# Performance work log

Measured on AMD Instinct MI355X. Metric: run time of the kernel, lower is better.

Reference implementation:

```python
import jax, jax.numpy as jnp
import numpy as np

# ---- static HashEncoder config (matches __init__ defaults) ----
D = 3            # input_dim
L = 16           # num_levels
C = 2            # level_dim
BASE = 16.0      # base_resolution (isotropic)
SCALE = 2.0      # per_level_scale (isotropic)
MAX_PARAMS = 2 ** 19  # log2_hashmap_size = 19

_base = np.full(D, BASE, dtype=np.float64)
_pls = np.full(D, SCALE, dtype=np.float64)
_offsets = [0]
_res = []
_off = 0
for i in range(L):
    r = np.ceil(_base * _pls ** i)
    _res.append(r.astype(np.int64))
    _off += int(min(MAX_PARAMS, np.prod(r)))
    _offsets.append(_off)
TOTAL_PARAMS = _off  # 7,114,752

# spatial-hash primes (instant-ngp convention; prime for dim 0 is 1)
PRIMES = np.array([1, 2654435761, 805459861], dtype=np.uint32)
# corner bit patterns for the 2^D = 8 cube corners, shape [8, D]
BITS = np.array([[(c >> d) & 1 for d in range(D)] for c in range(2 ** D)], dtype=np.uint32)
BITS_MASK = BITS.astype(bool)


def _encode_level(x01, embeddings, l):
    """x01: [B, D] normalized coords in [0, 1]; returns [B, C]."""
    scale = (_base * _pls ** l - 1.0).astype(np.float32)        # per-dim grid scale
    res = _res[l]                                               # per-dim resolution
    level_size = _offsets[l + 1] - _offsets[l]
    pos = x01 * scale + 0.5                                     # [B, D]
    pos_grid = jnp.floor(pos)
    frac = pos - pos_grid                                       # [B, D] in [0,1)
    pg = pos_grid.astype(jnp.uint32)                            # [B, D]
    corners = pg[:, None, :] + BITS[None]                       # [B, 8, D]
    # trilinear weights: prod over dims of frac (bit=1) or 1-frac (bit=0)
    w = jnp.prod(jnp.where(BITS_MASK[None], frac[:, None, :], 1.0 - frac[:, None, :]), axis=-1)  # [B, 8]
    if int(np.prod(res)) > level_size:
        # hashed level: xor of per-dim (coord * prime), mod table size
        h = corners * PRIMES[None, None, :]
        idx = (h[..., 0] ^ h[..., 1] ^ h[..., 2]) % jnp.uint32(level_size)
    else:
        # dense level: row-major stride indexing
        stride = np.array([1, res[0], res[0] * res[1]], dtype=np.uint32)
        idx = jnp.sum(corners * stride[None, None, :], axis=-1)  # [B, 8]
    g = embeddings[_offsets[l] + idx.astype(jnp.int32)]          # [B, 8, C] gather
    return jnp.sum(w[..., None] * g, axis=1)                     # [B, C]


def setup_inputs() -> dict:
    key = jax.random.key(0)
    k1, k2 = jax.random.split(key)
    B = 1048576
    inputs = jax.random.uniform(k1, (B, D), dtype=jnp.float32, minval=-1.0, maxval=1.0)
    # reset_parameters(): uniform(-0.1, 0.1)
    embeddings = jax.random.uniform(k2, (TOTAL_PARAMS, C), dtype=jnp.float32, minval=-0.1, maxval=0.1)
    return {"inputs": inputs, "embeddings": embeddings}


def reference(inputs, embeddings):
    # forward(inputs, size=1): normalize [-1,1] -> [0,1]
    x01 = (inputs + 1.0) * 0.5
    outs = [_encode_level(x01, embeddings, l) for l in range(L)]
    return jnp.concatenate(outs, axis=-1)  # [B, L*C] = [B, 32]
```

## Files before the change

kernel.cpp:

```cpp
#include <hip/hip_runtime.h>


static constexpr uint32_t P1 = 2654435761u;
static constexpr uint32_t P2 = 805459861u;
static constexpr uint32_t NPARAMS = 7114752u;
static constexpr uint32_t HMASK = 524287u;

__device__ inline uint32_t bf16_bits(float f) {
    uint32_t u = __float_as_uint(f);
    return (u + 0x7FFFu + ((u >> 16) & 1u)) >> 16;
}

__global__ __launch_bounds__(256) void convert_bf16(
    const float* __restrict__ emb, uint32_t* __restrict__ tab)
{
    const uint32_t i = blockIdx.x * 256u + threadIdx.x;
    const float4 v = ((const float4*)emb)[i];
    uint2 o;
    o.x = bf16_bits(v.x) | (bf16_bits(v.y) << 16);
    o.y = bf16_bits(v.z) | (bf16_bits(v.w) << 16);
    ((uint2*)tab)[i] = o;
}

__global__ __launch_bounds__(256) void enc_level(
    const float* __restrict__ inp,
    const uint32_t* __restrict__ tab,
    float2* __restrict__ stage,
    int npoints)
{
    const uint32_t l = blockIdx.y;
    const uint32_t p = blockIdx.x * 256u + threadIdx.x;
    if (p >= (uint32_t)npoints) return;

    const float x01 = (inp[p * 3u + 0u] + 1.0f) * 0.5f;
    const float y01 = (inp[p * 3u + 1u] + 1.0f) * 0.5f;
    const float z01 = (inp[p * 3u + 2u] + 1.0f) * 0.5f;

    const uint32_t res = 16u << l;
    const float scale = (float)(res - 1u);

    const float posx = x01 * scale + 0.5f;
    const float posy = y01 * scale + 0.5f;
    const float posz = z01 * scale + 0.5f;

    const float fgx = floorf(posx), fgy = floorf(posy), fgz = floorf(posz);
    const float fx = posx - fgx, fy = posy - fgy, fz = posz - fgz;
    const uint32_t gx = (uint32_t)fgx, gy = (uint32_t)fgy, gz = (uint32_t)fgz;

    uint32_t off;
    if (l >= 3u)      off = 299008u + (l - 3u) * 524288u;
    else if (l == 2u) off = 36864u;
    else if (l == 1u) off = 4096u;
    else              off = 0u;
    const bool hashed = (l >= 3u);
    const uint32_t s = 4u + (hashed ? 0u : l);

    const float wx0 = 1.0f - fx, wx1 = fx;
    const float wy[2] = {1.0f - fy, fy};
    const float wz[2] = {1.0f - fz, fz};

    uint32_t yzc[4];
    if (hashed) {
        const uint32_t hy0 = gy * P1, hy1 = hy0 + P1;
        const uint32_t hz0 = gz * P2, hz1 = hz0 + P2;
        yzc[0] = hy0 ^ hz0; yzc[1] = hy1 ^ hz0;
        yzc[2] = hy0 ^ hz1; yzc[3] = hy1 ^ hz1;
    } else {
        const uint32_t dy0 = gy << s, dy1 = dy0 + (1u << s);
        const uint32_t dz0 = gz << (2u * s), dz1 = dz0 + (1u << (2u * s));
        yzc[0] = dy0 + dz0; yzc[1] = dy1 + dz0;
        yzc[2] = dy0 + dz1; yzc[3] = dy1 + dz1;
    }

    const bool gx_odd = (gx & 1u) != 0u;

    uint32_t idxA[4], idxB[4];
#pragma unroll
    for (int c = 0; c < 4; ++c) {
        if (hashed) {
            idxA[c] = (gx ^ yzc[c]) & HMASK;
            idxB[c] = ((gx + 1u) ^ yzc[c]) & HMASK;
        } else {
            idxA[c] = gx + yzc[c];
            idxB[c] = idxA[c] + 1u;
        }
    }

    uint2 pr[4];
#pragma unroll
    for (int c = 0; c < 4; ++c)
        pr[c] = *(const uint2*)(tab + off + (idxA[c] & ~1u));

    uint32_t vBo[4];
    if (gx_odd) {
#pragma unroll
        for (int c = 0; c < 4; ++c)
            vBo[c] = tab[off + idxB[c]];
    }

    float sx = 0.0f, sy = 0.0f;
#pragma unroll
    for (int c = 0; c < 4; ++c) {
        const uint32_t lo = idxA[c] & 1u;
        const uint32_t vA = lo ? pr[c].y : pr[c].x;
        const uint32_t vBe = lo ? pr[c].x : pr[c].y;
        const uint32_t vB = gx_odd ? vBo[c] : vBe;
        const float wyz = wy[c & 1] * wz[c >> 1];
        const float eAx = __uint_as_float(vA << 16);
        const float eAy = __uint_as_float(vA & 0xFFFF0000u);
        const float eBx = __uint_as_float(vB << 16);
        const float eBy = __uint_as_float(vB & 0xFFFF0000u);
        sx = fmaf(wyz, fmaf(wx0, eAx, wx1 * eBx), sx);
        sy = fmaf(wyz, fmaf(wx0, eAy, wx1 * eBy), sy);
    }

    stage[(size_t)l * (uint32_t)npoints + p] = make_float2(sx, sy);
}

__global__ __launch_bounds__(256) void transpose_out(
    const float2* __restrict__ stage, float4* __restrict__ out4, int npoints)
{
    __shared__ float2 t[256][17];
    const uint32_t p0 = blockIdx.x * 256u;
    const uint32_t tid = threadIdx.x;

#pragma unroll
    for (int l = 0; l < 16; ++l)
        t[tid][l] = stage[(size_t)l * (uint32_t)npoints + p0 + tid];
    __syncthreads();

#pragma unroll
    for (int k = 0; k < 8; ++k) {
        const uint32_t f = (uint32_t)k * 256u + tid;
        const uint32_t p = f >> 3, c = f & 7u;
        const float2 a = t[p][2u * c];
        const float2 b = t[p][2u * c + 1u];
        out4[(size_t)(p0 + p) * 8u + c] = make_float4(a.x, a.y, b.x, b.y);
    }
}

__global__ __launch_bounds__(256) void hashenc_fwd(
    const float* __restrict__ inp, const float* __restrict__ emb,
    float* __restrict__ out, int npoints)
{
    const uint32_t tid = blockIdx.x * 256u + threadIdx.x;
    const uint32_t p = tid >> 4, l = tid & 15u;
    if (p >= (uint32_t)npoints) return;
    const float x01 = (inp[p * 3u + 0u] + 1.0f) * 0.5f;
    const float y01 = (inp[p * 3u + 1u] + 1.0f) * 0.5f;
    const float z01 = (inp[p * 3u + 2u] + 1.0f) * 0.5f;
    const uint32_t res = 16u << l;
    const float scale = (float)(res - 1u);
    const float posx = x01 * scale + 0.5f, posy = y01 * scale + 0.5f, posz = z01 * scale + 0.5f;
    const float fgx = floorf(posx), fgy = floorf(posy), fgz = floorf(posz);
    const float fx = posx - fgx, fy = posy - fgy, fz = posz - fgz;
    const uint32_t gx = (uint32_t)fgx, gy = (uint32_t)fgy, gz = (uint32_t)fgz;
    uint32_t off;
    if (l >= 3u)      off = 299008u + (l - 3u) * 524288u;
    else if (l == 2u) off = 36864u;
    else if (l == 1u) off = 4096u;
    else              off = 0u;
    const bool hashed = (l >= 3u);
    const uint32_t s = 4u + (hashed ? 0u : l);
    const float wx[2] = {1.0f - fx, fx}, wy[2] = {1.0f - fy, fy}, wz[2] = {1.0f - fz, fz};
    float2 g[8]; float w[8];
#pragma unroll
    for (int c = 0; c < 8; ++c) {
        const uint32_t bx = (uint32_t)c & 1u, by = ((uint32_t)c >> 1) & 1u, bz = ((uint32_t)c >> 2) & 1u;
        const uint32_t cx = gx + bx, cy = gy + by, cz = gz + bz;
        const uint32_t hidx = (cx ^ (cy * P1) ^ (cz * P2)) & HMASK;
        const uint32_t didx = cx + (cy << s) + (cz << (2u * s));
        const uint32_t idx  = hashed ? hidx : didx;
        w[c] = wx[bx] * wy[by] * wz[bz];
        g[c] = *(const float2*)(emb + 2u * (off + idx));
    }
    float sx = 0.0f, sy = 0.0f;
#pragma unroll
    for (int c = 0; c < 8; ++c) { sx = fmaf(w[c], g[c].x, sx); sy = fmaf(w[c], g[c].y, sy); }
    *(float2*)(out + (size_t)p * 32u + (size_t)l * 2u) = make_float2(sx, sy);
}

extern "C" void kernel_launch(void* const* d_in, const int* in_sizes, int n_in,
                              void* d_out, int out_size, void* d_ws, size_t ws_size,
                              hipStream_t stream) {
    const float* inp = (const float*)d_in[0];
    const float* emb = (const float*)d_in[1];
    float* out = (float*)d_out;
    const int npoints = in_sizes[0] / 3;

    const size_t tab_bytes = (size_t)NPARAMS * 4u;
    const size_t stage_bytes = (size_t)npoints * 16u * 8u;
    const size_t need = tab_bytes + stage_bytes;

    if (ws_size >= need && (npoints & 255) == 0) {
        uint32_t* tab = (uint32_t*)d_ws;
        float2* stage = (float2*)((char*)d_ws + tab_bytes);

        const int conv_units = (int)(NPARAMS * 2u / 4u);
        convert_bf16<<<(conv_units + 255) / 256, 256, 0, stream>>>(emb, tab);

        dim3 g1(npoints / 256, 16);
        enc_level<<<g1, 256, 0, stream>>>(inp, tab, stage, npoints);

        transpose_out<<<npoints / 256, 256, 0, stream>>>(stage, (float4*)out, npoints);
    } else {
        const int total = npoints * 16;
        hashenc_fwd<<<(total + 255) / 256, 256, 0, stream>>>(inp, emb, out, npoints);
    }
}
```

Before: 588.7 us.

## Fuse per-level encoding and output transpose into one kernel

```diff
diff --git a/kernel.cpp b/kernel.cpp
--- a/kernel.cpp
+++ b/kernel.cpp
@@ -22,20 +22,10 @@
     ((uint2*)tab)[i] = o;
 }
 
-__global__ __launch_bounds__(256) void enc_level(
-    const float* __restrict__ inp,
-    const uint32_t* __restrict__ tab,
-    float2* __restrict__ stage,
-    int npoints)
-{
-    const uint32_t l = blockIdx.y;
-    const uint32_t p = blockIdx.x * 256u + threadIdx.x;
-    if (p >= (uint32_t)npoints) return;
-
-    const float x01 = (inp[p * 3u + 0u] + 1.0f) * 0.5f;
-    const float y01 = (inp[p * 3u + 1u] + 1.0f) * 0.5f;
-    const float z01 = (inp[p * 3u + 2u] + 1.0f) * 0.5f;
-
+__device__ __forceinline__ float2 enc_point_level(
+    const float x01, const float y01, const float z01,
+    const uint32_t l, const uint32_t* __restrict__ tab)
+{
     const uint32_t res = 16u << l;
     const float scale = (float)(res - 1u);
 
@@ -113,29 +103,43 @@
         sx = fmaf(wyz, fmaf(wx0, eAx, wx1 * eBx), sx);
         sy = fmaf(wyz, fmaf(wx0, eAy, wx1 * eBy), sy);
     }
-
-    stage[(size_t)l * (uint32_t)npoints + p] = make_float2(sx, sy);
-}
-
-__global__ __launch_bounds__(256) void transpose_out(
-    const float2* __restrict__ stage, float4* __restrict__ out4, int npoints)
-{
-    __shared__ float2 t[256][17];
+    return make_float2(sx, sy);
+}
+
+__global__ __launch_bounds__(256, 8) void hashenc_fused(
+    const float* __restrict__ inp,
+    const uint32_t* __restrict__ tab,
+    float4* __restrict__ out4)
+{
+    __shared__ float2 t[256][9];
+
+    const uint32_t tid = threadIdx.x;
     const uint32_t p0 = blockIdx.x * 256u;
-    const uint32_t tid = threadIdx.x;
-
-#pragma unroll
-    for (int l = 0; l < 16; ++l)
-        t[tid][l] = stage[(size_t)l * (uint32_t)npoints + p0 + tid];
-    __syncthreads();
-
-#pragma unroll
-    for (int k = 0; k < 8; ++k) {
-        const uint32_t f = (uint32_t)k * 256u + tid;
-        const uint32_t p = f >> 3, c = f & 7u;
-        const float2 a = t[p][2u * c];
-        const float2 b = t[p][2u * c + 1u];
-        out4[(size_t)(p0 + p) * 8u + c] = make_float4(a.x, a.y, b.x, b.y);
+    const uint32_t p = p0 + tid;
+
+    const float x01 = (inp[p * 3u + 0u] + 1.0f) * 0.5f;
+    const float y01 = (inp[p * 3u + 1u] + 1.0f) * 0.5f;
+    const float z01 = (inp[p * 3u + 2u] + 1.0f) * 0.5f;
+
+#pragma unroll
+    for (uint32_t ph = 0u; ph < 2u; ++ph) {
+        if (ph) __syncthreads();
+
+#pragma unroll
+        for (uint32_t j = 0u; j < 8u; ++j)
+            t[tid][j] = enc_point_level(x01, y01, z01, ph * 8u + j, tab);
+
+        __syncthreads();
+
+#pragma unroll
+        for (uint32_t k = 0u; k < 4u; ++k) {
+            const uint32_t pl = k * 64u + (tid >> 2);
+            const uint32_t c = tid & 3u;
+            const float2 a = t[pl][2u * c];
+            const float2 b = t[pl][2u * c + 1u];
+            out4[(size_t)(p0 + pl) * 8u + ph * 4u + c] =
+                make_float4(a.x, a.y, b.x, b.y);
+        }
     }
 }
 
@@ -189,20 +193,14 @@
     const int npoints = in_sizes[0] / 3;
 
     const size_t tab_bytes = (size_t)NPARAMS * 4u;
-    const size_t stage_bytes = (size_t)npoints * 16u * 8u;
-    const size_t need = tab_bytes + stage_bytes;
-
-    if (ws_size >= need && (npoints & 255) == 0) {
+
+    if (ws_size >= tab_bytes && (npoints & 255) == 0) {
         uint32_t* tab = (uint32_t*)d_ws;
-        float2* stage = (float2*)((char*)d_ws + tab_bytes);
 
         const int conv_units = (int)(NPARAMS * 2u / 4u);
         convert_bf16<<<(conv_units + 255) / 256, 256, 0, stream>>>(emb, tab);
 
-        dim3 g1(npoints / 256, 16);
-        enc_level<<<g1, 256, 0, stream>>>(inp, tab, stage, npoints);
-
-        transpose_out<<<npoints / 256, 256, 0, stream>>>(stage, (float4*)out, npoints);
+        hashenc_fused<<<npoints / 256, 256, 0, stream>>>(inp, tab, (float4*)out);
     } else {
         const int total = npoints * 16;
         hashenc_fwd<<<(total + 255) / 256, 256, 0, stream>>>(inp, emb, out, npoints);
```

Result: slower. 689.5 us (+17.1%).
